# Optimization experiments

Hardware: AMD Instinct MI355X
Metric: run time of the kernel (lower is better)

## Reference

```python
import jax, jax.numpy as jnp
import numpy as np

# config
HIDDEN = 1024
NUM_EXPERTS = 16
TOP_K = 4
MOE_INTER = 512
NUM_SHARED = 2
SHARED_INTER = MOE_INTER * NUM_SHARED  # 1024
NORM_TOPK = True
ROUTED_SCALE = 1.0
NUM_TOKENS = 1024


def setup_inputs() -> dict:
    key = jax.random.key(0)
    ks = jax.random.split(key, 8)
    s = 0.02
    return {
        "hidden_states": jax.random.normal(ks[0], (NUM_TOKENS, HIDDEN), jnp.float32),
        # router (BailingMoEGate): weight [E, H], no bias
        "router_w": jax.random.normal(ks[1], (NUM_EXPERTS, HIDDEN), jnp.float32) * s,
        # routed experts: gate/up proj [E, H, I], down proj [E, I, H]
        "w_gate": jax.random.normal(ks[2], (NUM_EXPERTS, HIDDEN, MOE_INTER), jnp.float32) * s,
        "w_up": jax.random.normal(ks[3], (NUM_EXPERTS, HIDDEN, MOE_INTER), jnp.float32) * s,
        "w_down": jax.random.normal(ks[4], (NUM_EXPERTS, MOE_INTER, HIDDEN), jnp.float32) * s,
        # shared experts (BailingMoEMLP, merged gate_up): [H, 2*Is], [Is, H]
        "ws_gate_up": jax.random.normal(ks[5], (HIDDEN, 2 * SHARED_INTER), jnp.float32) * s,
        "ws_down": jax.random.normal(ks[6], (SHARED_INTER, HIDDEN), jnp.float32) * s,
    }


def _moe_forward(x, router_w, w_gate, w_up, w_down, ws_gate_up, ws_down):
    T = x.shape[0]
    # ---- router: logits -> softmax -> top-k (score_function='softmax', no bias)
    logits = jnp.einsum("th,eh->te", x, router_w)          # [T, E]
    probs = jax.nn.softmax(logits, axis=-1)
    topk_w, topk_idx = jax.lax.top_k(probs, TOP_K)         # [T, K]
    if NORM_TOPK:
        topk_w = topk_w / jnp.sum(topk_w, axis=-1, keepdims=True)
    topk_w = topk_w * ROUTED_SCALE
    # sparse combine weights [T, E] (zeros for non-selected experts)
    combine = jnp.zeros((T, NUM_EXPERTS), x.dtype).at[
        jnp.arange(T)[:, None], topk_idx
    ].set(topk_w.astype(x.dtype))
    # ---- routed experts: SiLU(x W_gate) * (x W_up) then W_down, weighted combine
    g = jnp.einsum("th,ehi->tei", x, w_gate)               # [T, E, I]
    u = jnp.einsum("th,ehi->tei", x, w_up)
    h = jax.nn.silu(g) * u
    routed = jnp.einsum("tei,eih,te->th", h, w_down, combine)
    # ---- shared experts (dense SwiGLU MLP)
    gu = x @ ws_gate_up                                    # [T, 2*Is]
    g_s, u_s = jnp.split(gu, 2, axis=-1)
    shared = (jax.nn.silu(g_s) * u_s) @ ws_down
    return routed + shared


def reference(hidden_states, router_w, w_gate, w_up, w_down, ws_gate_up, ws_down):
    return _moe_forward(hidden_states, router_w, w_gate, w_up, w_down,
                        ws_gate_up, ws_down)
```

## Files before the change

kernel.cpp:

```cpp
#include <hip/hip_runtime.h>
#include <stdint.h>


typedef __attribute__((ext_vector_type(8))) unsigned short ushort8;
typedef __attribute__((ext_vector_type(4))) float f32x4;
typedef __attribute__((ext_vector_type(8))) __bf16 bf16x8;

#define T_TOK 1024
#define HID   1024
#define NEXP  16
#define TOPK  4
#define MINTER 512
#define SINTER 1024

constexpr size_t OFF_COUNTS = 0;
constexpr size_t OFF_LIST   = 1024;
constexpr size_t OFF_WT     = OFF_LIST  + 65536;
constexpr size_t OFF_SLOT   = OFF_WT    + 65536;
constexpr size_t OFF_XB     = OFF_SLOT  + 65536;
constexpr size_t OFF_HS     = OFF_XB    + 2097152;
constexpr size_t OFF_HR     = OFF_HS    + 2097152;
constexpr size_t OFF_WGT    = OFF_HR    + 4194304;
constexpr size_t OFF_WUT    = OFF_WGT   + 16777216;
constexpr size_t OFF_WDT    = OFF_WUT   + 16777216;
constexpr size_t OFF_WSGUT  = OFF_WDT   + 16777216;
constexpr size_t OFF_WSDT   = OFF_WSGUT + 4194304;

__device__ __forceinline__ unsigned short f2bf(float f) {
  union { float f; uint32_t u; } v; v.f = f;
  uint32_t r = (v.u + 0x7FFFu + ((v.u >> 16) & 1u)) >> 16;
  return (unsigned short)r;
}
__device__ __forceinline__ bf16x8 as_bf16x8(ushort8 s) {
  union { ushort8 s; bf16x8 b; } u; u.s = s; return u.b;
}
__device__ __forceinline__ float silu(float g) {
  return g / (1.f + __expf(-g));
}

__global__ void init_kernel(int* counts) {
  if (threadIdx.x < NEXP) counts[threadIdx.x] = 0;
}

__global__ __launch_bounds__(64) void router_kernel(
    const float* __restrict__ x, const float* __restrict__ rw,
    int* counts, int* list, float* wt, int* slot) {
  const int t = blockIdx.x, l = threadIdx.x;
  float xv[16];
#pragma unroll
  for (int j = 0; j < 16; j++) xv[j] = x[t * HID + j * 64 + l];
  float p[NEXP];
#pragma unroll
  for (int e = 0; e < NEXP; e++) {
    float s = 0.f;
#pragma unroll
    for (int j = 0; j < 16; j++) s += xv[j] * rw[e * HID + j * 64 + l];
#pragma unroll
    for (int off = 32; off > 0; off >>= 1) s += __shfl_xor(s, off);
    p[e] = s;
  }
  float mx = p[0];
#pragma unroll
  for (int e = 1; e < NEXP; e++) mx = fmaxf(mx, p[e]);
  int idx[TOPK]; float w4[TOPK]; float wsum = 0.f; unsigned used = 0u;
#pragma unroll
  for (int k = 0; k < TOPK; k++) {
    float bv = -1e30f; int bi = 0;
#pragma unroll
    for (int e = 0; e < NEXP; e++)
      if (!((used >> e) & 1u) && p[e] > bv) { bv = p[e]; bi = e; }
    used |= 1u << bi;
    idx[k] = bi;
    w4[k] = __expf(p[bi] - mx);
    wsum += w4[k];
  }
  const float inv = 1.f / wsum;
  if (l < TOPK) {
    const int e = idx[l];
    const int pos = atomicAdd(&counts[e], 1);
    list[e * 1024 + pos] = t;
    wt[e * 1024 + pos]   = w4[l] * inv;
    slot[e * 1024 + pos] = t * TOPK + l;
  }
}

__global__ void convert_bf16_kernel(const float* __restrict__ src,
                                    unsigned short* __restrict__ dst, int n) {
  const int i = (blockIdx.x * blockDim.x + threadIdx.x) * 4;
  if (i + 3 < n) {
    const float4 v = *(const float4*)(src + i);
    dst[i + 0] = f2bf(v.x); dst[i + 1] = f2bf(v.y);
    dst[i + 2] = f2bf(v.z); dst[i + 3] = f2bf(v.w);
  }
}

__global__ __launch_bounds__(256) void transpose_cvt_kernel(
    const float* __restrict__ src, unsigned short* __restrict__ dst,
    int R, int C) {
  __shared__ float tile[32][33];
  const size_t bo = (size_t)blockIdx.z * R * C;
  src += bo; dst += bo;
  const int c0 = blockIdx.x * 32, r0 = blockIdx.y * 32;
  const int tx = threadIdx.x, ty = threadIdx.y;
#pragma unroll
  for (int i = 0; i < 4; i++)
    tile[ty + 8 * i][tx] = src[(size_t)(r0 + ty + 8 * i) * C + c0 + tx];
  __syncthreads();
#pragma unroll
  for (int i = 0; i < 4; i++)
    dst[(size_t)(c0 + ty + 8 * i) * R + r0 + tx] = f2bf(tile[tx][ty + 8 * i]);
}

#define LDK 40

__global__ __launch_bounds__(256) void shared_gu_kernel(
    const unsigned short* __restrict__ Xb, const unsigned short* __restrict__ WsguT,
    unsigned short* __restrict__ Hs) {
  __shared__ __align__(16) unsigned short sA[64 * LDK];
  __shared__ __align__(16) unsigned short sG[64 * LDK];
  __shared__ __align__(16) unsigned short sU[64 * LDK];
  const int tid = threadIdx.x, wave = tid >> 6, lane = tid & 63;
  const int m0 = blockIdx.y * 64, n0 = blockIdx.x * 64;
  const int sr = tid >> 2, skp = (tid & 3) * 8;
  const unsigned short* gA = Xb   + (size_t)(m0 + sr) * HID + skp;
  const unsigned short* gG = WsguT + (size_t)(n0 + sr) * HID + skp;
  const unsigned short* gU = WsguT + (size_t)(SINTER + n0 + sr) * HID + skp;
  const int sOff = sr * LDK + skp;
  const int aOff = (16 * wave + (lane & 15)) * LDK + (lane >> 4) * 8;
  int bOff[4];
#pragma unroll
  for (int c = 0; c < 4; c++) bOff[c] = (16 * c + (lane & 15)) * LDK + (lane >> 4) * 8;
  f32x4 accG[4], accU[4];
#pragma unroll
  for (int c = 0; c < 4; c++) { accG[c] = (f32x4){0.f,0.f,0.f,0.f}; accU[c] = (f32x4){0.f,0.f,0.f,0.f}; }
  for (int k0 = 0; k0 < HID; k0 += 32) {
    const ushort8 va = *(const ushort8*)(gA + k0);
    const ushort8 vg = *(const ushort8*)(gG + k0);
    const ushort8 vu = *(const ushort8*)(gU + k0);
    __syncthreads();
    *(ushort8*)(sA + sOff) = va;
    *(ushort8*)(sG + sOff) = vg;
    *(ushort8*)(sU + sOff) = vu;
    __syncthreads();
    const bf16x8 af = as_bf16x8(*(const ushort8*)(sA + aOff));
#pragma unroll
    for (int c = 0; c < 4; c++) {
      const bf16x8 gf = as_bf16x8(*(const ushort8*)(sG + bOff[c]));
      const bf16x8 uf = as_bf16x8(*(const ushort8*)(sU + bOff[c]));
      accG[c] = __builtin_amdgcn_mfma_f32_16x16x32_bf16(af, gf, accG[c], 0, 0, 0);
      accU[c] = __builtin_amdgcn_mfma_f32_16x16x32_bf16(af, uf, accU[c], 0, 0, 0);
    }
  }
  const int rb = 16 * wave + (lane >> 4) * 4, cb = lane & 15;
#pragma unroll
  for (int c = 0; c < 4; c++)
#pragma unroll
    for (int r = 0; r < 4; r++) {
      const float h = silu(accG[c][r]) * accU[c][r];
      Hs[(size_t)(m0 + rb + r) * SINTER + n0 + 16 * c + cb] = f2bf(h);
    }
}

__global__ __launch_bounds__(256) void shared_down_kernel(
    const unsigned short* __restrict__ Hs, const unsigned short* __restrict__ WsdT,
    float* __restrict__ out) {
  __shared__ __align__(16) unsigned short sA[64 * LDK];
  __shared__ __align__(16) unsigned short sB[64 * LDK];
  const int tid = threadIdx.x, wave = tid >> 6, lane = tid & 63;
  const int m0 = blockIdx.y * 64, n0 = blockIdx.x * 64;
  const int sr = tid >> 2, skp = (tid & 3) * 8;
  const unsigned short* gA = Hs   + (size_t)(m0 + sr) * SINTER + skp;
  const unsigned short* gB = WsdT + (size_t)(n0 + sr) * SINTER + skp;
  const int sOff = sr * LDK + skp;
  const int aOff = (16 * wave + (lane & 15)) * LDK + (lane >> 4) * 8;
  int bOff[4];
#pragma unroll
  for (int c = 0; c < 4; c++) bOff[c] = (16 * c + (lane & 15)) * LDK + (lane >> 4) * 8;
  f32x4 acc[4];
#pragma unroll
  for (int c = 0; c < 4; c++) acc[c] = (f32x4){0.f,0.f,0.f,0.f};
  for (int k0 = 0; k0 < SINTER; k0 += 32) {
    const ushort8 va = *(const ushort8*)(gA + k0);
    const ushort8 vb = *(const ushort8*)(gB + k0);
    __syncthreads();
    *(ushort8*)(sA + sOff) = va;
    *(ushort8*)(sB + sOff) = vb;
    __syncthreads();
    const bf16x8 af = as_bf16x8(*(const ushort8*)(sA + aOff));
#pragma unroll
    for (int c = 0; c < 4; c++) {
      const bf16x8 bfr = as_bf16x8(*(const ushort8*)(sB + bOff[c]));
      acc[c] = __builtin_amdgcn_mfma_f32_16x16x32_bf16(af, bfr, acc[c], 0, 0, 0);
    }
  }
  const int rb = 16 * wave + (lane >> 4) * 4, cb = lane & 15;
#pragma unroll
  for (int c = 0; c < 4; c++)
#pragma unroll
    for (int r = 0; r < 4; r++)
      out[(size_t)(m0 + rb + r) * HID + n0 + 16 * c + cb] = acc[c][r];
}

__global__ __launch_bounds__(256) void routed_gu_kernel(
    const unsigned short* __restrict__ Xb,
    const unsigned short* __restrict__ WgT, const unsigned short* __restrict__ WuT,
    const int* __restrict__ counts, const int* __restrict__ list,
    const int* __restrict__ slot, unsigned short* __restrict__ Hr) {
  const int e = blockIdx.z;
  const int cnt = counts[e];
  const int m0 = blockIdx.y * 64;
  if (m0 >= cnt) return;
  const int n0 = blockIdx.x * 64;
  __shared__ __align__(16) unsigned short sA[64 * LDK];
  __shared__ __align__(16) unsigned short sG[64 * LDK];
  __shared__ __align__(16) unsigned short sU[64 * LDK];
  const int tid = threadIdx.x, wave = tid >> 6, lane = tid & 63;
  const int sr = tid >> 2, skp = (tid & 3) * 8;
  int tok = list[e * 1024 + min(m0 + sr, cnt - 1)];
  tok = min(max(tok, 0), T_TOK - 1);
  const unsigned short* gA = Xb + (size_t)tok * HID + skp;
  const unsigned short* gG = WgT + (size_t)e * MINTER * HID + (size_t)(n0 + sr) * HID + skp;
  const unsigned short* gU = WuT + (size_t)e * MINTER * HID + (size_t)(n0 + sr) * HID + skp;
  const int sOff = sr * LDK + skp;
  const int aOff = (16 * wave + (lane & 15)) * LDK + (lane >> 4) * 8;
  int bOff[4];
#pragma unroll
  for (int c = 0; c < 4; c++) bOff[c] = (16 * c + (lane & 15)) * LDK + (lane >> 4) * 8;
  f32x4 accG[4], accU[4];
#pragma unroll
  for (int c = 0; c < 4; c++) { accG[c] = (f32x4){0.f,0.f,0.f,0.f}; accU[c] = (f32x4){0.f,0.f,0.f,0.f}; }
  for (int k0 = 0; k0 < HID; k0 += 32) {
    const ushort8 va = *(const ushort8*)(gA + k0);
    const ushort8 vg = *(const ushort8*)(gG + k0);
    const ushort8 vu = *(const ushort8*)(gU + k0);
    __syncthreads();
    *(ushort8*)(sA + sOff) = va;
    *(ushort8*)(sG + sOff) = vg;
    *(ushort8*)(sU + sOff) = vu;
    __syncthreads();
    const bf16x8 af = as_bf16x8(*(const ushort8*)(sA + aOff));
#pragma unroll
    for (int c = 0; c < 4; c++) {
      const bf16x8 gf = as_bf16x8(*(const ushort8*)(sG + bOff[c]));
      const bf16x8 uf = as_bf16x8(*(const ushort8*)(sU + bOff[c]));
      accG[c] = __builtin_amdgcn_mfma_f32_16x16x32_bf16(af, gf, accG[c], 0, 0, 0);
      accU[c] = __builtin_amdgcn_mfma_f32_16x16x32_bf16(af, uf, accU[c], 0, 0, 0);
    }
  }
  const int rb = 16 * wave + (lane >> 4) * 4, cb = lane & 15;
#pragma unroll
  for (int c = 0; c < 4; c++)
#pragma unroll
    for (int r = 0; r < 4; r++) {
      const int lrow = rb + r;
      if (m0 + lrow < cnt) {
        const int s = slot[e * 1024 + m0 + lrow];
        const float h = silu(accG[c][r]) * accU[c][r];
        Hr[(size_t)s * MINTER + n0 + 16 * c + cb] = f2bf(h);
      }
    }
}

__global__ __launch_bounds__(256) void routed_down_kernel(
    const unsigned short* __restrict__ Hr, const unsigned short* __restrict__ WdT,
    const int* __restrict__ counts, const int* __restrict__ list,
    const float* __restrict__ wt, const int* __restrict__ slot,
    float* __restrict__ out) {
  const int e = blockIdx.z;
  const int cnt = counts[e];
  const int m0 = blockIdx.y * 64;
  if (m0 >= cnt) return;
  const int n0 = blockIdx.x * 64;
  __shared__ __align__(16) unsigned short sA[64 * LDK];
  __shared__ __align__(16) unsigned short sB[64 * LDK];
  const int tid = threadIdx.x, wave = tid >> 6, lane = tid & 63;
  const int sr = tid >> 2, skp = (tid & 3) * 8;
  int s = slot[e * 1024 + min(m0 + sr, cnt - 1)];
  s = min(max(s, 0), T_TOK * TOPK - 1);
  const unsigned short* gA = Hr + (size_t)s * MINTER + skp;
  const unsigned short* gB = WdT + (size_t)e * HID * MINTER + (size_t)(n0 + sr) * MINTER + skp;
  const int sOff = sr * LDK + skp;
  const int aOff = (16 * wave + (lane & 15)) * LDK + (lane >> 4) * 8;
  int bOff[4];
#pragma unroll
  for (int c = 0; c < 4; c++) bOff[c] = (16 * c + (lane & 15)) * LDK + (lane >> 4) * 8;
  f32x4 acc[4];
#pragma unroll
  for (int c = 0; c < 4; c++) acc[c] = (f32x4){0.f,0.f,0.f,0.f};
  for (int k0 = 0; k0 < MINTER; k0 += 32) {
    const ushort8 va = *(const ushort8*)(gA + k0);
    const ushort8 vb = *(const ushort8*)(gB + k0);
    __syncthreads();
    *(ushort8*)(sA + sOff) = va;
    *(ushort8*)(sB + sOff) = vb;
    __syncthreads();
    const bf16x8 af = as_bf16x8(*(const ushort8*)(sA + aOff));
#pragma unroll
    for (int c = 0; c < 4; c++) {
      const bf16x8 bfr = as_bf16x8(*(const ushort8*)(sB + bOff[c]));
      acc[c] = __builtin_amdgcn_mfma_f32_16x16x32_bf16(af, bfr, acc[c], 0, 0, 0);
    }
  }
  const int rb = 16 * wave + (lane >> 4) * 4, cb = lane & 15;
#pragma unroll
  for (int c = 0; c < 4; c++)
#pragma unroll
    for (int r = 0; r < 4; r++) {
      const int lrow = rb + r;
      if (m0 + lrow < cnt) {
        const int t = list[e * 1024 + m0 + lrow];
        const float w = wt[e * 1024 + m0 + lrow];
        atomicAdd(out + (size_t)t * HID + n0 + 16 * c + cb, w * acc[c][r]);
      }
    }
}

extern "C" void kernel_launch(void* const* d_in, const int* in_sizes, int n_in,
                              void* d_out, int out_size, void* d_ws, size_t ws_size,
                              hipStream_t stream) {
  const float* x      = (const float*)d_in[0];
  const float* rw     = (const float*)d_in[1];
  const float* w_gate = (const float*)d_in[2];
  const float* w_up   = (const float*)d_in[3];
  const float* w_down = (const float*)d_in[4];
  const float* ws_gu  = (const float*)d_in[5];
  const float* ws_dn  = (const float*)d_in[6];
  float* out = (float*)d_out;
  char* ws = (char*)d_ws;

  int*   counts = (int*)  (ws + OFF_COUNTS);
  int*   list   = (int*)  (ws + OFF_LIST);
  float* wtbuf  = (float*)(ws + OFF_WT);
  int*   slot   = (int*)  (ws + OFF_SLOT);
  unsigned short* Xb    = (unsigned short*)(ws + OFF_XB);
  unsigned short* Hs    = (unsigned short*)(ws + OFF_HS);
  unsigned short* Hr    = (unsigned short*)(ws + OFF_HR);
  unsigned short* WgT   = (unsigned short*)(ws + OFF_WGT);
  unsigned short* WuT   = (unsigned short*)(ws + OFF_WUT);
  unsigned short* WdT   = (unsigned short*)(ws + OFF_WDT);
  unsigned short* WsguT = (unsigned short*)(ws + OFF_WSGUT);
  unsigned short* WsdT  = (unsigned short*)(ws + OFF_WSDT);

  init_kernel<<<1, 64, 0, stream>>>(counts);
  router_kernel<<<T_TOK, 64, 0, stream>>>(x, rw, counts, list, wtbuf, slot);
  convert_bf16_kernel<<<1024, 256, 0, stream>>>(x, Xb, T_TOK * HID);
  transpose_cvt_kernel<<<dim3(16, 32, 16), dim3(32, 8), 0, stream>>>(w_gate, WgT, HID, MINTER);
  transpose_cvt_kernel<<<dim3(16, 32, 16), dim3(32, 8), 0, stream>>>(w_up,   WuT, HID, MINTER);
  transpose_cvt_kernel<<<dim3(32, 16, 16), dim3(32, 8), 0, stream>>>(w_down, WdT, MINTER, HID);
  transpose_cvt_kernel<<<dim3(64, 32, 1),  dim3(32, 8), 0, stream>>>(ws_gu,  WsguT, HID, 2 * SINTER);
  transpose_cvt_kernel<<<dim3(32, 32, 1),  dim3(32, 8), 0, stream>>>(ws_dn,  WsdT, SINTER, HID);
  shared_gu_kernel<<<dim3(SINTER / 64, T_TOK / 64), 256, 0, stream>>>(Xb, WsguT, Hs);
  shared_down_kernel<<<dim3(HID / 64, T_TOK / 64), 256, 0, stream>>>(Hs, WsdT, out);
  routed_gu_kernel<<<dim3(MINTER / 64, T_TOK / 64, NEXP), 256, 0, stream>>>(
      Xb, WgT, WuT, counts, list, slot, Hr);
  routed_down_kernel<<<dim3(HID / 64, T_TOK / 64, NEXP), 256, 0, stream>>>(
      Hr, WdT, counts, list, wtbuf, slot, out);
  (void)in_sizes; (void)n_in; (void)out_size; (void)ws_size;
}
```

Measured before the change: 296.5 us.

## Merge shared and routed GEMMs into two large-tile fused kernels with deterministic combine

Replaces the four separate 64x64 GEMM kernels with two 128x(128/256) tile kernels. Each handles both the shared and the routed experts in one grid, uses direct global-to-LDS loads for weights, and uses an XOR-swizzled LDS layout. Routed hidden rows are packed contiguously per expert, with the routing weight applied in phase 1. The down projection writes per-slot fp32 rows into a reused workspace, and a separate combine kernel sums them instead of doing atomicAdd. The transpose kernel also moves to 64x64 tiles with vectorised loads and stores. This adds larger register and LDS footprints and an extra combine pass.

```diff
diff --git a/kernel.cpp b/kernel.cpp
--- a/kernel.cpp
+++ b/kernel.cpp
@@ -16,8 +16,8 @@
 constexpr size_t OFF_COUNTS = 0;
 constexpr size_t OFF_LIST   = 1024;
 constexpr size_t OFF_WT     = OFF_LIST  + 65536;
-constexpr size_t OFF_SLOT   = OFF_WT    + 65536;
-constexpr size_t OFF_XB     = OFF_SLOT  + 65536;
+constexpr size_t OFF_TIDX   = OFF_WT    + 65536;
+constexpr size_t OFF_XB     = OFF_TIDX  + 65536;
 constexpr size_t OFF_HS     = OFF_XB    + 2097152;
 constexpr size_t OFF_HR     = OFF_HS    + 2097152;
 constexpr size_t OFF_WGT    = OFF_HR    + 4194304;
@@ -25,6 +25,7 @@
 constexpr size_t OFF_WDT    = OFF_WUT   + 16777216;
 constexpr size_t OFF_WSGUT  = OFF_WDT   + 16777216;
 constexpr size_t OFF_WSDT   = OFF_WSGUT + 4194304;
+constexpr size_t OFF_ROUT   = OFF_WGT;
 
 __device__ __forceinline__ unsigned short f2bf(float f) {
   union { float f; uint32_t u; } v; v.f = f;
@@ -34,8 +35,12 @@
 __device__ __forceinline__ bf16x8 as_bf16x8(ushort8 s) {
   union { ushort8 s; bf16x8 b; } u; u.s = s; return u.b;
 }
-__device__ __forceinline__ float silu(float g) {
-  return g / (1.f + __expf(-g));
+__device__ __forceinline__ float silu(float g) { return g / (1.f + __expf(-g)); }
+
+__device__ __forceinline__ void glds16(const unsigned short* g, unsigned short* l) {
+  __builtin_amdgcn_global_load_lds(
+      (const __attribute__((address_space(1))) unsigned int*)g,
+      (__attribute__((address_space(3))) unsigned int*)l, 16, 0, 0);
 }
 
 __global__ void init_kernel(int* counts) {
@@ -44,7 +49,7 @@
 
 __global__ __launch_bounds__(64) void router_kernel(
     const float* __restrict__ x, const float* __restrict__ rw,
-    int* counts, int* list, float* wt, int* slot) {
+    int* counts, int* list, float* wt, int* tIdx) {
   const int t = blockIdx.x, l = threadIdx.x;
   float xv[16];
 #pragma unroll
@@ -80,7 +85,7 @@
     const int pos = atomicAdd(&counts[e], 1);
     list[e * 1024 + pos] = t;
     wt[e * 1024 + pos]   = w4[l] * inv;
-    slot[e * 1024 + pos] = t * TOPK + l;
+    tIdx[t * TOPK + l]   = (e << 10) | pos;
   }
 }
 
@@ -94,225 +99,291 @@
   }
 }
 
-__global__ __launch_bounds__(256) void transpose_cvt_kernel(
+__global__ __launch_bounds__(256) void transpose64_kernel(
     const float* __restrict__ src, unsigned short* __restrict__ dst,
     int R, int C) {
-  __shared__ float tile[32][33];
+  __shared__ float tile[64][65];
   const size_t bo = (size_t)blockIdx.z * R * C;
-  src += bo; dst += bo;
-  const int c0 = blockIdx.x * 32, r0 = blockIdx.y * 32;
-  const int tx = threadIdx.x, ty = threadIdx.y;
+  const int c0 = blockIdx.x * 64, r0 = blockIdx.y * 64, t = threadIdx.x;
+  {
+    const int r = t >> 4, c4 = (t & 15) * 4;
+#pragma unroll
+    for (int p = 0; p < 4; p++) {
+      const int rr = p * 16 + r;
+      const float4 v = *(const float4*)(src + bo + (size_t)(r0 + rr) * C + c0 + c4);
+      tile[rr][c4 + 0] = v.x; tile[rr][c4 + 1] = v.y;
+      tile[rr][c4 + 2] = v.z; tile[rr][c4 + 3] = v.w;
+    }
+  }
+  __syncthreads();
+  {
+    const int c = t >> 2, rb = (t & 3) * 16;
+#pragma unroll
+    for (int s = 0; s < 4; s++) {
+      const int rr = rb + 4 * s;
+      union { unsigned short u[4]; uint2 v; } pk;
+#pragma unroll
+      for (int i = 0; i < 4; i++) pk.u[i] = f2bf(tile[rr + i][c]);
+      *(uint2*)(dst + bo + (size_t)(c0 + c) * R + r0 + rr) = pk.v;
+    }
+  }
+}
+
+__global__ __launch_bounds__(256, 2) void phase1_kernel(
+    const unsigned short* __restrict__ Xb,
+    const unsigned short* __restrict__ WgT,
+    const unsigned short* __restrict__ WuT,
+    const unsigned short* __restrict__ WsguT,
+    const int* __restrict__ counts, const int* __restrict__ list,
+    const float* __restrict__ wt,
+    unsigned short* __restrict__ Hr,
+    unsigned short* __restrict__ Hs) {
+  const int z = blockIdx.z, x = blockIdx.x, y = blockIdx.y;
+  const bool routed = (z < NEXP);
+  int cnt = 0, base = 0;
+  if (routed) {
+    if (x >= 4) return;
+    cnt = counts[z];
+    if (y * 128 >= cnt) return;
+#pragma unroll
+    for (int i = 0; i < NEXP; i++) base += (i < z) ? counts[i] : 0;
+  }
+  __shared__ __align__(16) unsigned short sA[128 * 64];
+  __shared__ __align__(16) unsigned short sB[256 * 64];
+  const int tid = threadIdx.x, w = tid >> 6, l = tid & 63;
+  const int wm = w >> 1, wn = w & 1, m0 = y * 128;
+
+  const int ar = tid >> 1;
+  const unsigned short* aRow;
+  if (routed) {
+    const int pos = min(m0 + ar, cnt - 1);
+    aRow = Xb + (size_t)list[z * 1024 + pos] * HID;
+  } else {
+    aRow = Xb + (size_t)(m0 + ar) * HID;
+  }
+  const unsigned short* aptr[4];
+  int aoff[4];
+#pragma unroll
+  for (int c = 0; c < 4; c++) {
+    const int p = (tid & 1) * 4 + c;
+    aptr[c] = aRow + ((p ^ (ar & 7)) * 8);
+    aoff[c] = ar * 64 + p * 8;
+  }
+  const unsigned short* bptr[8];
+#pragma unroll
+  for (int i = 0; i < 8; i++) {
+    const int R = 64 * w + 8 * i + (l >> 3);
+    const int g = (l & 7) ^ (R & 7);
+    const unsigned short* rowp;
+    if (routed) {
+      const int col = x * 128 + (R & 127);
+      rowp = ((R >> 7) ? WuT : WgT) + (size_t)z * MINTER * HID + (size_t)col * HID;
+    } else {
+      const int col = x * 128 + (R & 127);
+      rowp = WsguT + (size_t)((R >> 7) * SINTER + col) * HID;
+    }
+    bptr[i] = rowp + g * 8;
+  }
+
+  f32x4 accG[4][4], accU[4][4];
 #pragma unroll
   for (int i = 0; i < 4; i++)
-    tile[ty + 8 * i][tx] = src[(size_t)(r0 + ty + 8 * i) * C + c0 + tx];
+#pragma unroll
+    for (int j = 0; j < 4; j++) {
+      accG[i][j] = (f32x4){0.f, 0.f, 0.f, 0.f};
+      accU[i][j] = (f32x4){0.f, 0.f, 0.f, 0.f};
+    }
+
+  for (int k0 = 0; k0 < HID; k0 += 64) {
+    ushort8 av[4];
+#pragma unroll
+    for (int c = 0; c < 4; c++) av[c] = *(const ushort8*)(aptr[c] + k0);
+    __syncthreads();
+#pragma unroll
+    for (int c = 0; c < 4; c++) *(ushort8*)(sA + aoff[c]) = av[c];
+#pragma unroll
+    for (int i = 0; i < 8; i++)
+      glds16(bptr[i] + k0, sB + (64 * w + 8 * i) * 64);
+    __syncthreads();
+#pragma unroll
+    for (int h = 0; h < 2; h++) {
+      const int pc = ((h * 4 + (l >> 4)) ^ (l & 7)) * 8;
+      bf16x8 af[4];
+#pragma unroll
+      for (int i = 0; i < 4; i++)
+        af[i] = as_bf16x8(*(const ushort8*)(sA + (wm * 64 + 16 * i + (l & 15)) * 64 + pc));
+#pragma unroll
+      for (int j = 0; j < 4; j++) {
+        const int Rg = wn * 64 + 16 * j + (l & 15);
+        const bf16x8 gf = as_bf16x8(*(const ushort8*)(sB + Rg * 64 + pc));
+        const bf16x8 uf = as_bf16x8(*(const ushort8*)(sB + (128 + Rg) * 64 + pc));
+#pragma unroll
+        for (int i = 0; i < 4; i++) {
+          accG[i][j] = __builtin_amdgcn_mfma_f32_16x16x32_bf16(af[i], gf, accG[i][j], 0, 0, 0);
+          accU[i][j] = __builtin_amdgcn_mfma_f32_16x16x32_bf16(af[i], uf, accU[i][j], 0, 0, 0);
+        }
+      }
+    }
+  }
+
+#pragma unroll
+  for (int i = 0; i < 4; i++)
+#pragma unroll
+    for (int r = 0; r < 4; r++) {
+      const int row = wm * 64 + 16 * i + (l >> 4) * 4 + r;
+      const int grow = m0 + row;
+      if (routed) {
+        if (grow < cnt) {
+          const float wrow = wt[z * 1024 + grow];
+#pragma unroll
+          for (int j = 0; j < 4; j++) {
+            const int col = x * 128 + wn * 64 + 16 * j + (l & 15);
+            const float h = silu(accG[i][j][r]) * accU[i][j][r] * wrow;
+            Hr[(size_t)(base + grow) * MINTER + col] = f2bf(h);
+          }
+        }
+      } else {
+#pragma unroll
+        for (int j = 0; j < 4; j++) {
+          const int col = x * 128 + wn * 64 + 16 * j + (l & 15);
+          const float h = silu(accG[i][j][r]) * accU[i][j][r];
+          Hs[(size_t)grow * SINTER + col] = f2bf(h);
+        }
+      }
+    }
+}
+
+__global__ __launch_bounds__(256, 2) void phase2_kernel(
+    const unsigned short* __restrict__ Hr, const unsigned short* __restrict__ Hs,
+    const unsigned short* __restrict__ WdT,
+    const unsigned short* __restrict__ WsdT,
+    const int* __restrict__ counts,
+    float* __restrict__ Rout,
+    float* __restrict__ out) {
+  const int z = blockIdx.z, x = blockIdx.x, y = blockIdx.y;
+  const bool routed = (z < NEXP);
+  int cnt = 0, base = 0, kdim;
+  if (routed) {
+    cnt = counts[z];
+    if (y * 128 >= cnt) return;
+#pragma unroll
+    for (int i = 0; i < NEXP; i++) base += (i < z) ? counts[i] : 0;
+    kdim = MINTER;
+  } else {
+    kdim = SINTER;
+  }
+  __shared__ __align__(16) unsigned short sA[128 * 64];
+  __shared__ __align__(16) unsigned short sB[256 * 64];
+  const int tid = threadIdx.x, w = tid >> 6, l = tid & 63;
+  const int wm = w >> 1, wn = w & 1, m0 = y * 128;
+
+  const int ar = tid >> 1;
+  const unsigned short* aRow;
+  if (routed) {
+    const int pos = min(m0 + ar, cnt - 1);
+    aRow = Hr + (size_t)(base + pos) * MINTER;
+  } else {
+    aRow = Hs + (size_t)(m0 + ar) * SINTER;
+  }
+  const unsigned short* aptr[4];
+  int aoff[4];
+#pragma unroll
+  for (int c = 0; c < 4; c++) {
+    const int p = (tid & 1) * 4 + c;
+    aptr[c] = aRow + ((p ^ (ar & 7)) * 8);
+    aoff[c] = ar * 64 + p * 8;
+  }
+  const unsigned short* bptr[8];
+#pragma unroll
+  for (int i = 0; i < 8; i++) {
+    const int R = 64 * w + 8 * i + (l >> 3);
+    const int g = (l & 7) ^ (R & 7);
+    const int col = x * 256 + R;
+    const unsigned short* rowp =
+        routed ? (WdT + (size_t)z * HID * MINTER + (size_t)col * MINTER)
+               : (WsdT + (size_t)col * SINTER);
+    bptr[i] = rowp + g * 8;
+  }
+
+  f32x4 acc[4][8];
+#pragma unroll
+  for (int i = 0; i < 4; i++)
+#pragma unroll
+    for (int j = 0; j < 8; j++) acc[i][j] = (f32x4){0.f, 0.f, 0.f, 0.f};
+
+  for (int k0 = 0; k0 < kdim; k0 += 64) {
+    ushort8 av[4];
+#pragma unroll
+    for (int c = 0; c < 4; c++) av[c] = *(const ushort8*)(aptr[c] + k0);
+    __syncthreads();
+#pragma unroll
+    for (int c = 0; c < 4; c++) *(ushort8*)(sA + aoff[c]) = av[c];
+#pragma unroll
+    for (int i = 0; i < 8; i++)
+      glds16(bptr[i] + k0, sB + (64 * w + 8 * i) * 64);
+    __syncthreads();
+#pragma unroll
+    for (int h = 0; h < 2; h++) {
+      const int pc = ((h * 4 + (l >> 4)) ^ (l & 7)) * 8;
+      bf16x8 af[4];
+#pragma unroll
+      for (int i = 0; i < 4; i++)
+        af[i] = as_bf16x8(*(const ushort8*)(sA + (wm * 64 + 16 * i + (l & 15)) * 64 + pc));
+#pragma unroll
+      for (int j = 0; j < 8; j++) {
+        const int Rb = wn * 128 + 16 * j + (l & 15);
+        const bf16x8 bfv = as_bf16x8(*(const ushort8*)(sB + Rb * 64 + pc));
+#pragma unroll
+        for (int i = 0; i < 4; i++)
+          acc[i][j] = __builtin_amdgcn_mfma_f32_16x16x32_bf16(af[i], bfv, acc[i][j], 0, 0, 0);
+      }
+    }
+  }
+
+#pragma unroll
+  for (int i = 0; i < 4; i++)
+#pragma unroll
+    for (int r = 0; r < 4; r++) {
+      const int row = wm * 64 + 16 * i + (l >> 4) * 4 + r;
+      const int grow = m0 + row;
+      if (routed) {
+        if (grow < cnt) {
+#pragma unroll
+          for (int j = 0; j < 8; j++) {
+            const int col = x * 256 + wn * 128 + 16 * j + (l & 15);
+            Rout[(size_t)(base + grow) * HID + col] = acc[i][j][r];
+          }
+        }
+      } else {
+#pragma unroll
+        for (int j = 0; j < 8; j++) {
+          const int col = x * 256 + wn * 128 + 16 * j + (l & 15);
+          out[(size_t)grow * HID + col] = acc[i][j][r];
+        }
+      }
+    }
+}
+
+__global__ __launch_bounds__(256) void combine_kernel(
+    const float* __restrict__ Rout, const int* __restrict__ counts,
+    const int* __restrict__ tIdx, float* __restrict__ out) {
+  __shared__ int sb[NEXP];
+  if (threadIdx.x == 0) {
+    int s = 0;
+#pragma unroll
+    for (int e = 0; e < NEXP; e++) { sb[e] = s; s += counts[e]; }
+  }
   __syncthreads();
-#pragma unroll
-  for (int i = 0; i < 4; i++)
-    dst[(size_t)(c0 + ty + 8 * i) * R + r0 + tx] = f2bf(tile[tx][ty + 8 * i]);
-}
-
-#define LDK 40
-
-__global__ __launch_bounds__(256) void shared_gu_kernel(
-    const unsigned short* __restrict__ Xb, const unsigned short* __restrict__ WsguT,
-    unsigned short* __restrict__ Hs) {
-  __shared__ __align__(16) unsigned short sA[64 * LDK];
-  __shared__ __align__(16) unsigned short sG[64 * LDK];
-  __shared__ __align__(16) unsigned short sU[64 * LDK];
-  const int tid = threadIdx.x, wave = tid >> 6, lane = tid & 63;
-  const int m0 = blockIdx.y * 64, n0 = blockIdx.x * 64;
-  const int sr = tid >> 2, skp = (tid & 3) * 8;
-  const unsigned short* gA = Xb   + (size_t)(m0 + sr) * HID + skp;
-  const unsigned short* gG = WsguT + (size_t)(n0 + sr) * HID + skp;
-  const unsigned short* gU = WsguT + (size_t)(SINTER + n0 + sr) * HID + skp;
-  const int sOff = sr * LDK + skp;
-  const int aOff = (16 * wave + (lane & 15)) * LDK + (lane >> 4) * 8;
-  int bOff[4];
-#pragma unroll
-  for (int c = 0; c < 4; c++) bOff[c] = (16 * c + (lane & 15)) * LDK + (lane >> 4) * 8;
-  f32x4 accG[4], accU[4];
-#pragma unroll
-  for (int c = 0; c < 4; c++) { accG[c] = (f32x4){0.f,0.f,0.f,0.f}; accU[c] = (f32x4){0.f,0.f,0.f,0.f}; }
-  for (int k0 = 0; k0 < HID; k0 += 32) {
-    const ushort8 va = *(const ushort8*)(gA + k0);
-    const ushort8 vg = *(const ushort8*)(gG + k0);
-    const ushort8 vu = *(const ushort8*)(gU + k0);
-    __syncthreads();
-    *(ushort8*)(sA + sOff) = va;
-    *(ushort8*)(sG + sOff) = vg;
-    *(ushort8*)(sU + sOff) = vu;
-    __syncthreads();
-    const bf16x8 af = as_bf16x8(*(const ushort8*)(sA + aOff));
-#pragma unroll
-    for (int c = 0; c < 4; c++) {
-      const bf16x8 gf = as_bf16x8(*(const ushort8*)(sG + bOff[c]));
-      const bf16x8 uf = as_bf16x8(*(const ushort8*)(sU + bOff[c]));
-      accG[c] = __builtin_amdgcn_mfma_f32_16x16x32_bf16(af, gf, accG[c], 0, 0, 0);
-      accU[c] = __builtin_amdgcn_mfma_f32_16x16x32_bf16(af, uf, accU[c], 0, 0, 0);
-    }
-  }
-  const int rb = 16 * wave + (lane >> 4) * 4, cb = lane & 15;
-#pragma unroll
-  for (int c = 0; c < 4; c++)
-#pragma unroll
-    for (int r = 0; r < 4; r++) {
-      const float h = silu(accG[c][r]) * accU[c][r];
-      Hs[(size_t)(m0 + rb + r) * SINTER + n0 + 16 * c + cb] = f2bf(h);
-    }
-}
-
-__global__ __launch_bounds__(256) void shared_down_kernel(
-    const unsigned short* __restrict__ Hs, const unsigned short* __restrict__ WsdT,
-    float* __restrict__ out) {
-  __shared__ __align__(16) unsigned short sA[64 * LDK];
-  __shared__ __align__(16) unsigned short sB[64 * LDK];
-  const int tid = threadIdx.x, wave = tid >> 6, lane = tid & 63;
-  const int m0 = blockIdx.y * 64, n0 = blockIdx.x * 64;
-  const int sr = tid >> 2, skp = (tid & 3) * 8;
-  const unsigned short* gA = Hs   + (size_t)(m0 + sr) * SINTER + skp;
-  const unsigned short* gB = WsdT + (size_t)(n0 + sr) * SINTER + skp;
-  const int sOff = sr * LDK + skp;
-  const int aOff = (16 * wave + (lane & 15)) * LDK + (lane >> 4) * 8;
-  int bOff[4];
-#pragma unroll
-  for (int c = 0; c < 4; c++) bOff[c] = (16 * c + (lane & 15)) * LDK + (lane >> 4) * 8;
-  f32x4 acc[4];
-#pragma unroll
-  for (int c = 0; c < 4; c++) acc[c] = (f32x4){0.f,0.f,0.f,0.f};
-  for (int k0 = 0; k0 < SINTER; k0 += 32) {
-    const ushort8 va = *(const ushort8*)(gA + k0);
-    const ushort8 vb = *(const ushort8*)(gB + k0);
-    __syncthreads();
-    *(ushort8*)(sA + sOff) = va;
-    *(ushort8*)(sB + sOff) = vb;
-    __syncthreads();
-    const bf16x8 af = as_bf16x8(*(const ushort8*)(sA + aOff));
-#pragma unroll
-    for (int c = 0; c < 4; c++) {
-      const bf16x8 bfr = as_bf16x8(*(const ushort8*)(sB + bOff[c]));
-      acc[c] = __builtin_amdgcn_mfma_f32_16x16x32_bf16(af, bfr, acc[c], 0, 0, 0);
-    }
-  }
-  const int rb = 16 * wave + (lane >> 4) * 4, cb = lane & 15;
-#pragma unroll
-  for (int c = 0; c < 4; c++)
-#pragma unroll
-    for (int r = 0; r < 4; r++)
-      out[(size_t)(m0 + rb + r) * HID + n0 + 16 * c + cb] = acc[c][r];
-}
-
-__global__ __launch_bounds__(256) void routed_gu_kernel(
-    const unsigned short* __restrict__ Xb,
-    const unsigned short* __restrict__ WgT, const unsigned short* __restrict__ WuT,
-    const int* __restrict__ counts, const int* __restrict__ list,
-    const int* __restrict__ slot, unsigned short* __restrict__ Hr) {
-  const int e = blockIdx.z;
-  const int cnt = counts[e];
-  const int m0 = blockIdx.y * 64;
-  if (m0 >= cnt) return;
-  const int n0 = blockIdx.x * 64;
-  __shared__ __align__(16) unsigned short sA[64 * LDK];
-  __shared__ __align__(16) unsigned short sG[64 * LDK];
-  __shared__ __align__(16) unsigned short sU[64 * LDK];
-  const int tid = threadIdx.x, wave = tid >> 6, lane = tid & 63;
-  const int sr = tid >> 2, skp = (tid & 3) * 8;
-  int tok = list[e * 1024 + min(m0 + sr, cnt - 1)];
-  tok = min(max(tok, 0), T_TOK - 1);
-  const unsigned short* gA = Xb + (size_t)tok * HID + skp;
-  const unsigned short* gG = WgT + (size_t)e * MINTER * HID + (size_t)(n0 + sr) * HID + skp;
-  const unsigned short* gU = WuT + (size_t)e * MINTER * HID + (size_t)(n0 + sr) * HID + skp;
-  const int sOff = sr * LDK + skp;
-  const int aOff = (16 * wave + (lane & 15)) * LDK + (lane >> 4) * 8;
-  int bOff[4];
-#pragma unroll
-  for (int c = 0; c < 4; c++) bOff[c] = (16 * c + (lane & 15)) * LDK + (lane >> 4) * 8;
-  f32x4 accG[4], accU[4];
-#pragma unroll
-  for (int c = 0; c < 4; c++) { accG[c] = (f32x4){0.f,0.f,0.f,0.f}; accU[c] = (f32x4){0.f,0.f,0.f,0.f}; }
-  for (int k0 = 0; k0 < HID; k0 += 32) {
-    const ushort8 va = *(const ushort8*)(gA + k0);
-    const ushort8 vg = *(const ushort8*)(gG + k0);
-    const ushort8 vu = *(const ushort8*)(gU + k0);
-    __syncthreads();
-    *(ushort8*)(sA + sOff) = va;
-    *(ushort8*)(sG + sOff) = vg;
-    *(ushort8*)(sU + sOff) = vu;
-    __syncthreads();
-    const bf16x8 af = as_bf16x8(*(const ushort8*)(sA + aOff));
-#pragma unroll
-    for (int c = 0; c < 4; c++) {
-      const bf16x8 gf = as_bf16x8(*(const ushort8*)(sG + bOff[c]));
-      const bf16x8 uf = as_bf16x8(*(const ushort8*)(sU + bOff[c]));
-      accG[c] = __builtin_amdgcn_mfma_f32_16x16x32_bf16(af, gf, accG[c], 0, 0, 0);
-      accU[c] = __builtin_amdgcn_mfma_f32_16x16x32_bf16(af, uf, accU[c], 0, 0, 0);
-    }
-  }
-  const int rb = 16 * wave + (lane >> 4) * 4, cb = lane & 15;
-#pragma unroll
-  for (int c = 0; c < 4; c++)
-#pragma unroll
-    for (int r = 0; r < 4; r++) {
-      const int lrow = rb + r;
-      if (m0 + lrow < cnt) {
-        const int s = slot[e * 1024 + m0 + lrow];
-        const float h = silu(accG[c][r]) * accU[c][r];
-        Hr[(size_t)s * MINTER + n0 + 16 * c + cb] = f2bf(h);
-      }
-    }
-}
-
-__global__ __launch_bounds__(256) void routed_down_kernel(
-    const unsigned short* __restrict__ Hr, const unsigned short* __restrict__ WdT,
-    const int* __restrict__ counts, const int* __restrict__ list,
-    const float* __restrict__ wt, const int* __restrict__ slot,
-    float* __restrict__ out) {
-  const int e = blockIdx.z;
-  const int cnt = counts[e];
-  const int m0 = blockIdx.y * 64;
-  if (m0 >= cnt) return;
-  const int n0 = blockIdx.x * 64;
-  __shared__ __align__(16) unsigned short sA[64 * LDK];
-  __shared__ __align__(16) unsigned short sB[64 * LDK];
-  const int tid = threadIdx.x, wave = tid >> 6, lane = tid & 63;
-  const int sr = tid >> 2, skp = (tid & 3) * 8;
-  int s = slot[e * 1024 + min(m0 + sr, cnt - 1)];
-  s = min(max(s, 0), T_TOK * TOPK - 1);
-  const unsigned short* gA = Hr + (size_t)s * MINTER + skp;
-  const unsigned short* gB = WdT + (size_t)e * HID * MINTER + (size_t)(n0 + sr) * MINTER + skp;
-  const int sOff = sr * LDK + skp;
-  const int aOff = (16 * wave + (lane & 15)) * LDK + (lane >> 4) * 8;
-  int bOff[4];
-#pragma unroll
-  for (int c = 0; c < 4; c++) bOff[c] = (16 * c + (lane & 15)) * LDK + (lane >> 4) * 8;
-  f32x4 acc[4];
-#pragma unroll
-  for (int c = 0; c < 4; c++) acc[c] = (f32x4){0.f,0.f,0.f,0.f};
-  for (int k0 = 0; k0 < MINTER; k0 += 32) {
-    const ushort8 va = *(const ushort8*)(gA + k0);
-    const ushort8 vb = *(const ushort8*)(gB + k0);
-    __syncthreads();
-    *(ushort8*)(sA + sOff) = va;
-    *(ushort8*)(sB + sOff) = vb;
-    __syncthreads();
-    const bf16x8 af = as_bf16x8(*(const ushort8*)(sA + aOff));
-#pragma unroll
-    for (int c = 0; c < 4; c++) {
-      const bf16x8 bfr = as_bf16x8(*(const ushort8*)(sB + bOff[c]));
-      acc[c] = __builtin_amdgcn_mfma_f32_16x16x32_bf16(af, bfr, acc[c], 0, 0, 0);
-    }
-  }
-  const int rb = 16 * wave + (lane >> 4) * 4, cb = lane & 15;
-#pragma unroll
-  for (int c = 0; c < 4; c++)
-#pragma unroll
-    for (int r = 0; r < 4; r++) {
-      const int lrow = rb + r;
-      if (m0 + lrow < cnt) {
-        const int t = list[e * 1024 + m0 + lrow];
-        const float w = wt[e * 1024 + m0 + lrow];
-        atomicAdd(out + (size_t)t * HID + n0 + 16 * c + cb, w * acc[c][r]);
-      }
-    }
+  const int t = blockIdx.x, c4 = threadIdx.x * 4;
+  float4 o = *(const float4*)(out + (size_t)t * HID + c4);
+#pragma unroll
+  for (int k = 0; k < TOPK; k++) {
+    const int v = tIdx[t * TOPK + k];
+    const int row = sb[v >> 10] + (v & 1023);
+    const float4 rv = *(const float4*)(Rout + (size_t)row * HID + c4);
+    o.x += rv.x; o.y += rv.y; o.z += rv.z; o.w += rv.w;
+  }
+  *(float4*)(out + (size_t)t * HID + c4) = o;
 }
 
 extern "C" void kernel_launch(void* const* d_in, const int* in_sizes, int n_in,
@@ -331,7 +402,7 @@
   int*   counts = (int*)  (ws + OFF_COUNTS);
   int*   list   = (int*)  (ws + OFF_LIST);
   float* wtbuf  = (float*)(ws + OFF_WT);
-  int*   slot   = (int*)  (ws + OFF_SLOT);
+  int*   tIdx   = (int*)  (ws + OFF_TIDX);
   unsigned short* Xb    = (unsigned short*)(ws + OFF_XB);
   unsigned short* Hs    = (unsigned short*)(ws + OFF_HS);
   unsigned short* Hr    = (unsigned short*)(ws + OFF_HR);
@@ -340,20 +411,20 @@
   unsigned short* WdT   = (unsigned short*)(ws + OFF_WDT);
   unsigned short* WsguT = (unsigned short*)(ws + OFF_WSGUT);
   unsigned short* WsdT  = (unsigned short*)(ws + OFF_WSDT);
+  float* Rout = (float*)(ws + OFF_ROUT);
 
   init_kernel<<<1, 64, 0, stream>>>(counts);
-  router_kernel<<<T_TOK, 64, 0, stream>>>(x, rw, counts, list, wtbuf, slot);
+  router_kernel<<<T_TOK, 64, 0, stream>>>(x, rw, counts, list, wtbuf, tIdx);
   convert_bf16_kernel<<<1024, 256, 0, stream>>>(x, Xb, T_TOK * HID);
-  transpose_cvt_kernel<<<dim3(16, 32, 16), dim3(32, 8), 0, stream>>>(w_gate, WgT, HID, MINTER);
-  transpose_cvt_kernel<<<dim3(16, 32, 16), dim3(32, 8), 0, stream>>>(w_up,   WuT, HID, MINTER);
-  transpose_cvt_kernel<<<dim3(32, 16, 16), dim3(32, 8), 0, stream>>>(w_down, WdT, MINTER, HID);
-  transpose_cvt_kernel<<<dim3(64, 32, 1),  dim3(32, 8), 0, stream>>>(ws_gu,  WsguT, HID, 2 * SINTER);
-  transpose_cvt_kernel<<<dim3(32, 32, 1),  dim3(32, 8), 0, stream>>>(ws_dn,  WsdT, SINTER, HID);
-  shared_gu_kernel<<<dim3(SINTER / 64, T_TOK / 64), 256, 0, stream>>>(Xb, WsguT, Hs);
-  shared_down_kernel<<<dim3(HID / 64, T_TOK / 64), 256, 0, stream>>>(Hs, WsdT, out);
-  routed_gu_kernel<<<dim3(MINTER / 64, T_TOK / 64, NEXP), 256, 0, stream>>>(
-      Xb, WgT, WuT, counts, list, slot, Hr);
-  routed_down_kernel<<<dim3(HID / 64, T_TOK / 64, NEXP), 256, 0, stream>>>(
-      Hr, WdT, counts, list, wtbuf, slot, out);
+  transpose64_kernel<<<dim3(8, 16, 16), 256, 0, stream>>>(w_gate, WgT, HID, MINTER);
+  transpose64_kernel<<<dim3(8, 16, 16), 256, 0, stream>>>(w_up,   WuT, HID, MINTER);
+  transpose64_kernel<<<dim3(16, 8, 16), 256, 0, stream>>>(w_down, WdT, MINTER, HID);
+  transpose64_kernel<<<dim3(32, 16, 1), 256, 0, stream>>>(ws_gu,  WsguT, HID, 2 * SINTER);
+  transpose64_kernel<<<dim3(16, 16, 1), 256, 0, stream>>>(ws_dn,  WsdT, SINTER, HID);
+  phase1_kernel<<<dim3(8, 8, 17), 256, 0, stream>>>(
+      Xb, WgT, WuT, WsguT, counts, list, wtbuf, Hr, Hs);
+  phase2_kernel<<<dim3(4, 8, 17), 256, 0, stream>>>(
+      Hr, Hs, WdT, WsdT, counts, Rout, out);
+  combine_kernel<<<T_TOK, 256, 0, stream>>>(Rout, counts, tIdx, out);
   (void)in_sizes; (void)n_in; (void)out_size; (void)ws_size;
 }
```

After: 301.5 us. No clear change (+1.7%).
